# Optimization experiments

Measured on AMD Instinct MI355X. Metric: run time of the kernel, lower is better.

## Reference

```python
import jax, jax.numpy as jnp
import numpy as np

B, S, E, H, MAXLEN = 2, 2048, 1024, 16, 2048


def _level_indices(seq_len: int, base: int = 2) -> np.ndarray:
    """Vectorized version of get_level_index_weak over the full (target, source) grid.
    indices[t, s] = min(level, 2) for s < t, else 0. Runs in O(log S) passes."""
    tt = np.broadcast_to(np.arange(seq_len)[:, None], (seq_len, seq_len)).astype(np.int64).copy()
    ss = np.broadcast_to(np.arange(seq_len)[None, :], (seq_len, seq_len)).astype(np.int64).copy()
    res = np.zeros((seq_len, seq_len), np.int64)
    done = ~(ss < tt)  # only source < target positions get a level; rest stay 0
    while not done.all():
        l = np.floor(np.log2(np.maximum(tt, 1).astype(np.float64))).astype(np.int64)
        v = (np.int64(1) << l)
        hit = (~done) & (ss < v)
        res[hit] = l[hit] + 1
        done |= hit
        step = ~done
        tt[step] -= v[step]
        ss[step] -= v[step]
    return np.minimum(res, 2).astype(np.int32)


def setup_inputs() -> dict:
    key = jax.random.key(0)
    ks = jax.random.split(key, 10)
    sc = 0.02
    return {
        "x": jax.random.normal(ks[0], (B, S, E), dtype=jnp.float32),
        "attention_mask": jax.random.randint(ks[1], (B, S), 0, 2, dtype=jnp.int32),
        "level_indices": jnp.asarray(_level_indices(S, 2)),
        "Wq": jax.random.normal(ks[2], (E, E), dtype=jnp.float32) * sc,
        "bq": jnp.zeros((E,), jnp.float32),
        "Wk": jax.random.normal(ks[3], (E, E), dtype=jnp.float32) * sc,
        "bk": jnp.zeros((E,), jnp.float32),
        "Wv": jax.random.normal(ks[4], (E, E), dtype=jnp.float32) * sc,
        "bv": jnp.zeros((E,), jnp.float32),
        "hier": jax.random.normal(ks[5], (MAXLEN, H, 3), dtype=jnp.float32),
        "Wo": jax.random.normal(ks[6], (E, E), dtype=jnp.float32) * sc,
        "bo": jnp.zeros((E,), jnp.float32),
    }


def reference(x, attention_mask, level_indices, Wq, bq, Wk, bk, Wv, bv, hier, Wo, bo):
    b, s, e = x.shape
    h = hier.shape[1]
    dh = e // h
    # q/k are computed by the original module but never used; kept for fidelity (zero grads).
    q = x @ Wq.T + bq
    k = x @ Wk.T + bk
    v = (x @ Wv.T + bv).reshape(b, s, h, dh).transpose(0, 2, 1, 3)  # [B,H,S,Dh]
    lev = level_indices[:s, :s]  # [S,S] int, values in {0,1,2}
    # Faithful torch.gather semantics: weights[b,h,i,j] = hier[b, h, lev[i,j]]
    w3 = hier[:b]                      # [B,H,3]
    weights = w3[:, :, lev]            # [B,H,S,S]
    decay = jnp.power(jnp.float32(0.5), lev.astype(x.dtype))  # [S,S]
    weights = weights * decay
    weights = weights / (jnp.sum(weights, axis=-1, keepdims=True) + 1e-8)
    weights = jnp.where(attention_mask[:, None, None, :] == 0, jnp.float32(0.0), weights)
    out = jnp.einsum('bhij,bhjd->bhid', weights, v)  # [B,H,S,Dh]
    out = out.transpose(0, 2, 1, 3).reshape(b, s, e)
    return out @ Wo.T + bo
```

## Files before the change

kernel.cpp:

```cpp
#include <hip/hip_runtime.h>
#include <cstdint>
#include <cstddef>

constexpr int Sn = 2048;
constexpr int En = 1024;
constexpr int Bn = 2;
constexpr int Hn = 16;
constexpr int CHUNK = 64;
constexpr int NCH = Sn / CHUNK;
constexpr int Mtot = Bn * Sn;
constexpr int GCH = Mtot / CHUNK;
constexpr int KB = En / 32;

typedef __bf16 bf16x8 __attribute__((ext_vector_type(8)));
typedef float  f32x4  __attribute__((ext_vector_type(4)));

__device__ __forceinline__ unsigned short f2bf(float f) {
    union { float f; uint32_t u; } v; v.f = f;
    const uint32_t u = v.u;
    return (unsigned short)((u + 0x7fffu + ((u >> 16) & 1u)) >> 16);
}
__device__ __forceinline__ float bf2f(unsigned short s) {
    union { uint32_t u; float f; } v; v.u = (uint32_t)s << 16; return v.f;
}

__device__ __forceinline__ size_t swz_idx(int r, int c, int kb ) {
    const int blk = (r >> 4) * kb + (c >> 5);
    return (size_t)blk * 512 + (((r & 15) + (((c >> 3) & 3) << 4)) << 3) + (c & 7);
}

constexpr int XN = Bn * Sn * En;
constexpr int WN = En * En;

__global__ __launch_bounds__(256)
void cast3(const float* __restrict__ x, const float* __restrict__ Wv,
           const float* __restrict__ Wo, unsigned short* __restrict__ xb,
           unsigned short* __restrict__ Wvb, unsigned short* __restrict__ Wob)
{
    const int i = (blockIdx.x * 256 + threadIdx.x) * 4;
    const float* src; unsigned short* dst; int off;
    if (i < XN)           { src = x;  dst = xb;  off = i; }
    else if (i < XN + WN) { src = Wv; dst = Wvb; off = i - XN; }
    else                  { src = Wo; dst = Wob; off = i - XN - WN; }
    const float4 v = *(const float4*)(src + off);
    ushort4 o;
    o.x = f2bf(v.x); o.y = f2bf(v.y); o.z = f2bf(v.z); o.w = f2bf(v.w);
    const int r = off >> 10, c = off & 1023;
    *(ushort4*)(dst + swz_idx(r, c, KB)) = o;
}

template<bool APPLY_MASK, bool OUT_BF16, bool FUSE_CSUM>
__global__ __launch_bounds__(256)
void gemm_flat(const unsigned short* __restrict__ A, const unsigned short* __restrict__ Bw,
               const float* __restrict__ bias, const int* __restrict__ mask,
               void* __restrict__ Cv, float* __restrict__ csum)
{
    const int tid  = threadIdx.x;
    const int lane = tid & 63;
    const int wv   = tid >> 6;
    const int wr   = wv >> 1;
    const int wc   = wv & 1;
    const int id   = blockIdx.y * 16 + blockIdx.x;
    const int xcd  = id & 7;
    const int slot = id >> 3;
    const int by   = xcd * 4 + (slot >> 4);
    const int bx   = slot & 15;
    const int bm   = by * 128;
    const int bn   = bx * 64;
    const int m16  = lane & 15;
    const int kq   = lane >> 4;

    f32x4 acc[4][2] = {};

    const int rb = by * 8 + wr * 4;
    const int cb = bx * 4 + wc * 2;
    const unsigned short* aBase = A  + (size_t)rb * KB * 512 + lane * 8;
    const unsigned short* bBase = Bw + (size_t)cb * KB * 512 + lane * 8;

#pragma unroll 4
    for (int kc = 0; kc < KB; ++kc) {
        bf16x8 af0 = *(const bf16x8*)(aBase + (size_t)(0 * KB + kc) * 512);
        bf16x8 af1 = *(const bf16x8*)(aBase + (size_t)(1 * KB + kc) * 512);
        bf16x8 af2 = *(const bf16x8*)(aBase + (size_t)(2 * KB + kc) * 512);
        bf16x8 af3 = *(const bf16x8*)(aBase + (size_t)(3 * KB + kc) * 512);
        bf16x8 bf0 = *(const bf16x8*)(bBase + (size_t)(0 * KB + kc) * 512);
        bf16x8 bf1 = *(const bf16x8*)(bBase + (size_t)(1 * KB + kc) * 512);
        acc[0][0] = __builtin_amdgcn_mfma_f32_16x16x32_bf16(af0, bf0, acc[0][0], 0, 0, 0);
        acc[0][1] = __builtin_amdgcn_mfma_f32_16x16x32_bf16(af0, bf1, acc[0][1], 0, 0, 0);
        acc[1][0] = __builtin_amdgcn_mfma_f32_16x16x32_bf16(af1, bf0, acc[1][0], 0, 0, 0);
        acc[1][1] = __builtin_amdgcn_mfma_f32_16x16x32_bf16(af1, bf1, acc[1][1], 0, 0, 0);
        acc[2][0] = __builtin_amdgcn_mfma_f32_16x16x32_bf16(af2, bf0, acc[2][0], 0, 0, 0);
        acc[2][1] = __builtin_amdgcn_mfma_f32_16x16x32_bf16(af2, bf1, acc[2][1], 0, 0, 0);
        acc[3][0] = __builtin_amdgcn_mfma_f32_16x16x32_bf16(af3, bf0, acc[3][0], 0, 0, 0);
        acc[3][1] = __builtin_amdgcn_mfma_f32_16x16x32_bf16(af3, bf1, acc[3][1], 0, 0, 0);
    }

    float colsum[2] = {0.0f, 0.0f};
#pragma unroll
    for (int i = 0; i < 4; ++i) {
        const int r0 = bm + wr * 64 + i * 16 + kq * 4;
#pragma unroll
        for (int j = 0; j < 2; ++j) {
            const int c0 = bn + wc * 32 + j * 16 + m16;
            const float bcol = bias[c0];
#pragma unroll
            for (int r = 0; r < 4; ++r) {
                const int row = r0 + r;
                float val = acc[i][j][r] + bcol;
                if (APPLY_MASK) val = (mask[row] == 0) ? 0.0f : val;
                if (FUSE_CSUM) colsum[j] += val;
                if (OUT_BF16)
                    ((unsigned short*)Cv)[(size_t)row * En + c0] = f2bf(val);
                else
                    ((float*)Cv)[(size_t)row * En + c0] = val;
            }
        }
    }

    if (FUSE_CSUM) {
        const int gc = 2 * by + wr;
#pragma unroll
        for (int j = 0; j < 2; ++j) {
            float s = colsum[j];
            s += __shfl_xor(s, 16, 64);
            s += __shfl_xor(s, 32, 64);
            if (kq == 0)
                csum[(size_t)gc * En + bn + wc * 32 + j * 16 + m16] = s;
        }
    }
}

__global__ __launch_bounds__(256)
void combine(const unsigned short* __restrict__ vm, const float* __restrict__ csum,
             const float* __restrict__ hier, unsigned short* __restrict__ opre)
{
    const int e = blockIdx.x * 256 + threadIdx.x;
    const int c = blockIdx.y;
    const int b = blockIdx.z;
    const int h = e >> 6;

    const float w0 = hier[((size_t)b * Hn + h) * 3 + 0];
    const float w1 = hier[((size_t)b * Hn + h) * 3 + 1] * 0.5f;
    const float w2 = hier[((size_t)b * Hn + h) * 3 + 2] * 0.25f;

    float run = 0.0f, T = 0.0f;
    const int g0 = b * NCH;
    for (int c2 = 0; c2 < NCH; ++c2) {
        const float v = csum[(size_t)(g0 + c2) * En + e];
        if (c2 < c) run += v;
        T += v;
    }

    const int ecol  = (e >> 5);
    const int elane = ((e >> 3) & 3) << 4;
    const int epos  = e & 7;

    float prev = 0.0f;
    const size_t base = ((size_t)b * Sn + c * CHUNK) * En + e;

    for (int t = 0; t < CHUNK; ++t) {
        const int i = c * CHUNK + t;
        const float cur = bf2f(vm[base + (size_t)t * En]);
        float num, Z;
        if (i & 1) {
            num = w2 * (run - prev) + w1 * prev + w0 * (T - run);
            Z = (float)(i - 1) * w2 + w1 + (float)(Sn - i) * w0 + 1e-8f;
        } else {
            num = w2 * run + w0 * (T - run);
            Z = (float)i * w2 + (float)(Sn - i) * w0 + 1e-8f;
        }
        const int gi = b * Sn + i;
        const size_t di = (size_t)((gi >> 4) * KB + ecol) * 512
                        + ((((gi & 15) + elane)) << 3) + epos;
        opre[di] = f2bf(num / Z);
        run += cur;
        prev = cur;
    }
}

extern "C" void kernel_launch(void* const* d_in, const int* in_sizes, int n_in,
                              void* d_out, int out_size, void* d_ws, size_t ws_size,
                              hipStream_t stream)
{
    const float* x    = (const float*)d_in[0];
    const int*   mask = (const int*)d_in[1];
    const float* Wv   = (const float*)d_in[7];
    const float* bv   = (const float*)d_in[8];
    const float* hier = (const float*)d_in[9];
    const float* Wo   = (const float*)d_in[10];
    const float* bo   = (const float*)d_in[11];
    float* out = (float*)d_out;

    char* ws = (char*)d_ws;
    unsigned short* xb    = (unsigned short*)ws;  ws += (size_t)Mtot * En * 2;
    unsigned short* Wvb   = (unsigned short*)ws;  ws += (size_t)En * En * 2;
    unsigned short* Wob   = (unsigned short*)ws;  ws += (size_t)En * En * 2;
    unsigned short* vmb   = (unsigned short*)ws;  ws += (size_t)Mtot * En * 2;
    float*          csum  = (float*)ws;           ws += (size_t)GCH * En * 4;
    unsigned short* opreb = (unsigned short*)ws;  ws += (size_t)Mtot * En * 2;

    dim3 threads(256);

    cast3<<<dim3((XN + 2 * WN) / 1024), threads, 0, stream>>>(x, Wv, Wo, xb, Wvb, Wob);

    dim3 gemm_grid(16, 32);

    gemm_flat<true, true, true><<<gemm_grid, threads, 0, stream>>>(xb, Wvb, bv, mask, vmb, csum);
    combine<<<dim3(En / 256, NCH, Bn), threads, 0, stream>>>(vmb, csum, hier, opreb);
    gemm_flat<false, false, false><<<gemm_grid, threads, 0, stream>>>(opreb, Wob, bo, nullptr, out, nullptr);
}
```

Before: 180.3 us.

## Stage GEMM tiles through LDS with register prefetch, drop swizzled layout

Both GEMMs stop reading pre-swizzled fragments straight from global memory. They now load 128-wide K slabs from row-major bf16 buffers into registers, stage them into shared memory in MFMA fragment order, and prefetch the next slab while computing the current one. The cast and combine kernels now write plain row-major output instead of the swizzled layout. The aim is to share A/B tiles across waves and hide global latency, at the cost of extra barriers and 48KB of LDS per block, which may reduce occupancy.

```diff
diff --git a/kernel.cpp b/kernel.cpp
--- a/kernel.cpp
+++ b/kernel.cpp
@@ -10,7 +10,6 @@
 constexpr int NCH = Sn / CHUNK;
 constexpr int Mtot = Bn * Sn;
 constexpr int GCH = Mtot / CHUNK;
-constexpr int KB = En / 32;
 
 typedef __bf16 bf16x8 __attribute__((ext_vector_type(8)));
 typedef float  f32x4  __attribute__((ext_vector_type(4)));
@@ -22,11 +21,6 @@
 }
 __device__ __forceinline__ float bf2f(unsigned short s) {
     union { uint32_t u; float f; } v; v.u = (uint32_t)s << 16; return v.f;
-}
-
-__device__ __forceinline__ size_t swz_idx(int r, int c, int kb ) {
-    const int blk = (r >> 4) * kb + (c >> 5);
-    return (size_t)blk * 512 + (((r & 15) + (((c >> 3) & 3) << 4)) << 3) + (c & 7);
 }
 
 constexpr int XN = Bn * Sn * En;
@@ -45,16 +39,58 @@
     const float4 v = *(const float4*)(src + off);
     ushort4 o;
     o.x = f2bf(v.x); o.y = f2bf(v.y); o.z = f2bf(v.z); o.w = f2bf(v.w);
-    const int r = off >> 10, c = off & 1023;
-    *(ushort4*)(dst + swz_idx(r, c, KB)) = o;
-}
+    *(ushort4*)(dst + off) = o;
+}
+
+#define LOAD12(S, k0)                                \
+    S##a0 = *(const uint4*)(gA0 + (k0));             \
+    S##a1 = *(const uint4*)(gA0 + (k0) + 32);        \
+    S##a2 = *(const uint4*)(gA0 + (k0) + 64);        \
+    S##a3 = *(const uint4*)(gA0 + (k0) + 96);        \
+    S##a4 = *(const uint4*)(gA1 + (k0));             \
+    S##a5 = *(const uint4*)(gA1 + (k0) + 32);        \
+    S##a6 = *(const uint4*)(gA1 + (k0) + 64);        \
+    S##a7 = *(const uint4*)(gA1 + (k0) + 96);        \
+    S##b0 = *(const uint4*)(gB0 + (k0));             \
+    S##b1 = *(const uint4*)(gB0 + (k0) + 32);        \
+    S##b2 = *(const uint4*)(gB0 + (k0) + 64);        \
+    S##b3 = *(const uint4*)(gB0 + (k0) + 96);
+
+#define STORE12(S)                                   \
+    *lA0 = S##a0; *lA1 = S##a1; *lA2 = S##a2; *lA3 = S##a3; \
+    *lA4 = S##a4; *lA5 = S##a5; *lA6 = S##a6; *lA7 = S##a7; \
+    *lB0 = S##b0; *lB1 = S##b1; *lB2 = S##b2; *lB3 = S##b3;
+
+#define COMPUTE128()                                                                           \
+    {                                                                                          \
+        _Pragma("unroll")                                                                      \
+        for (int kh = 0; kh < 4; ++kh) {                                                       \
+            bf16x8 af0 = *(const bf16x8*)&As[((wr * 4 + 0) * 4 + kh) * 512 + lane * 8];        \
+            bf16x8 af1 = *(const bf16x8*)&As[((wr * 4 + 1) * 4 + kh) * 512 + lane * 8];        \
+            bf16x8 af2 = *(const bf16x8*)&As[((wr * 4 + 2) * 4 + kh) * 512 + lane * 8];        \
+            bf16x8 af3 = *(const bf16x8*)&As[((wr * 4 + 3) * 4 + kh) * 512 + lane * 8];        \
+            bf16x8 bf0 = *(const bf16x8*)&Bs[((wc * 2 + 0) * 4 + kh) * 512 + lane * 8];        \
+            bf16x8 bf1 = *(const bf16x8*)&Bs[((wc * 2 + 1) * 4 + kh) * 512 + lane * 8];        \
+            acc[0][0] = __builtin_amdgcn_mfma_f32_16x16x32_bf16(af0, bf0, acc[0][0], 0, 0, 0); \
+            acc[0][1] = __builtin_amdgcn_mfma_f32_16x16x32_bf16(af0, bf1, acc[0][1], 0, 0, 0); \
+            acc[1][0] = __builtin_amdgcn_mfma_f32_16x16x32_bf16(af1, bf0, acc[1][0], 0, 0, 0); \
+            acc[1][1] = __builtin_amdgcn_mfma_f32_16x16x32_bf16(af1, bf1, acc[1][1], 0, 0, 0); \
+            acc[2][0] = __builtin_amdgcn_mfma_f32_16x16x32_bf16(af2, bf0, acc[2][0], 0, 0, 0); \
+            acc[2][1] = __builtin_amdgcn_mfma_f32_16x16x32_bf16(af2, bf1, acc[2][1], 0, 0, 0); \
+            acc[3][0] = __builtin_amdgcn_mfma_f32_16x16x32_bf16(af3, bf0, acc[3][0], 0, 0, 0); \
+            acc[3][1] = __builtin_amdgcn_mfma_f32_16x16x32_bf16(af3, bf1, acc[3][1], 0, 0, 0); \
+        }                                                                                      \
+    }
 
 template<bool APPLY_MASK, bool OUT_BF16, bool FUSE_CSUM>
 __global__ __launch_bounds__(256)
-void gemm_flat(const unsigned short* __restrict__ A, const unsigned short* __restrict__ Bw,
-               const float* __restrict__ bias, const int* __restrict__ mask,
-               void* __restrict__ Cv, float* __restrict__ csum)
-{
+void gemm_bk128(const unsigned short* __restrict__ A, const unsigned short* __restrict__ Bw,
+                const float* __restrict__ bias, const int* __restrict__ mask,
+                void* __restrict__ Cv, float* __restrict__ csum)
+{
+    __shared__ __align__(16) unsigned short As[128 * 128];
+    __shared__ __align__(16) unsigned short Bs[64 * 128];
+
     const int tid  = threadIdx.x;
     const int lane = tid & 63;
     const int wv   = tid >> 6;
@@ -72,27 +108,41 @@
 
     f32x4 acc[4][2] = {};
 
-    const int rb = by * 8 + wr * 4;
-    const int cb = bx * 4 + wc * 2;
-    const unsigned short* aBase = A  + (size_t)rb * KB * 512 + lane * 8;
-    const unsigned short* bBase = Bw + (size_t)cb * KB * 512 + lane * 8;
-
-#pragma unroll 4
-    for (int kc = 0; kc < KB; ++kc) {
-        bf16x8 af0 = *(const bf16x8*)(aBase + (size_t)(0 * KB + kc) * 512);
-        bf16x8 af1 = *(const bf16x8*)(aBase + (size_t)(1 * KB + kc) * 512);
-        bf16x8 af2 = *(const bf16x8*)(aBase + (size_t)(2 * KB + kc) * 512);
-        bf16x8 af3 = *(const bf16x8*)(aBase + (size_t)(3 * KB + kc) * 512);
-        bf16x8 bf0 = *(const bf16x8*)(bBase + (size_t)(0 * KB + kc) * 512);
-        bf16x8 bf1 = *(const bf16x8*)(bBase + (size_t)(1 * KB + kc) * 512);
-        acc[0][0] = __builtin_amdgcn_mfma_f32_16x16x32_bf16(af0, bf0, acc[0][0], 0, 0, 0);
-        acc[0][1] = __builtin_amdgcn_mfma_f32_16x16x32_bf16(af0, bf1, acc[0][1], 0, 0, 0);
-        acc[1][0] = __builtin_amdgcn_mfma_f32_16x16x32_bf16(af1, bf0, acc[1][0], 0, 0, 0);
-        acc[1][1] = __builtin_amdgcn_mfma_f32_16x16x32_bf16(af1, bf1, acc[1][1], 0, 0, 0);
-        acc[2][0] = __builtin_amdgcn_mfma_f32_16x16x32_bf16(af2, bf0, acc[2][0], 0, 0, 0);
-        acc[2][1] = __builtin_amdgcn_mfma_f32_16x16x32_bf16(af2, bf1, acc[2][1], 0, 0, 0);
-        acc[3][0] = __builtin_amdgcn_mfma_f32_16x16x32_bf16(af3, bf0, acc[3][0], 0, 0, 0);
-        acc[3][1] = __builtin_amdgcn_mfma_f32_16x16x32_bf16(af3, bf1, acc[3][1], 0, 0, 0);
+    const int rg0 = 2 * wv, rg1 = 2 * wv + 1;
+    const unsigned short* gA0 = A  + (size_t)(bm + 16 * rg0 + m16) * En + kq * 8;
+    const unsigned short* gA1 = A  + (size_t)(bm + 16 * rg1 + m16) * En + kq * 8;
+    const unsigned short* gB0 = Bw + (size_t)(bn + 16 * wv  + m16) * En + kq * 8;
+    uint4* lA0 = (uint4*)&As[(rg0 * 4 + 0) * 512 + lane * 8];
+    uint4* lA1 = (uint4*)&As[(rg0 * 4 + 1) * 512 + lane * 8];
+    uint4* lA2 = (uint4*)&As[(rg0 * 4 + 2) * 512 + lane * 8];
+    uint4* lA3 = (uint4*)&As[(rg0 * 4 + 3) * 512 + lane * 8];
+    uint4* lA4 = (uint4*)&As[(rg1 * 4 + 0) * 512 + lane * 8];
+    uint4* lA5 = (uint4*)&As[(rg1 * 4 + 1) * 512 + lane * 8];
+    uint4* lA6 = (uint4*)&As[(rg1 * 4 + 2) * 512 + lane * 8];
+    uint4* lA7 = (uint4*)&As[(rg1 * 4 + 3) * 512 + lane * 8];
+    uint4* lB0 = (uint4*)&Bs[(wv * 4 + 0) * 512 + lane * 8];
+    uint4* lB1 = (uint4*)&Bs[(wv * 4 + 1) * 512 + lane * 8];
+    uint4* lB2 = (uint4*)&Bs[(wv * 4 + 2) * 512 + lane * 8];
+    uint4* lB3 = (uint4*)&Bs[(wv * 4 + 3) * 512 + lane * 8];
+
+    uint4 pa0, pa1, pa2, pa3, pa4, pa5, pa6, pa7, pb0, pb1, pb2, pb3;
+    uint4 qa0, qa1, qa2, qa3, qa4, qa5, qa6, qa7, qb0, qb1, qb2, qb3;
+
+    LOAD12(p, 0);
+#pragma unroll 1
+    for (int it = 0; it < 4; ++it) {
+        const int kbase = it * 256;
+        __syncthreads();
+        STORE12(p);
+        __syncthreads();
+        LOAD12(q, kbase + 128);
+        COMPUTE128();
+
+        __syncthreads();
+        STORE12(q);
+        __syncthreads();
+        if (it < 3) { LOAD12(p, kbase + 256); }
+        COMPUTE128();
     }
 
     float colsum[2] = {0.0f, 0.0f};
@@ -151,10 +201,6 @@
         T += v;
     }
 
-    const int ecol  = (e >> 5);
-    const int elane = ((e >> 3) & 3) << 4;
-    const int epos  = e & 7;
-
     float prev = 0.0f;
     const size_t base = ((size_t)b * Sn + c * CHUNK) * En + e;
 
@@ -169,10 +215,7 @@
             num = w2 * run + w0 * (T - run);
             Z = (float)i * w2 + (float)(Sn - i) * w0 + 1e-8f;
         }
-        const int gi = b * Sn + i;
-        const size_t di = (size_t)((gi >> 4) * KB + ecol) * 512
-                        + ((((gi & 15) + elane)) << 3) + epos;
-        opre[di] = f2bf(num / Z);
+        opre[base + (size_t)t * En] = f2bf(num / Z);
         run += cur;
         prev = cur;
     }
@@ -205,7 +248,7 @@
 
     dim3 gemm_grid(16, 32);
 
-    gemm_flat<true, true, true><<<gemm_grid, threads, 0, stream>>>(xb, Wvb, bv, mask, vmb, csum);
+    gemm_bk128<true, true, true><<<gemm_grid, threads, 0, stream>>>(xb, Wvb, bv, mask, vmb, csum);
     combine<<<dim3(En / 256, NCH, Bn), threads, 0, stream>>>(vmb, csum, hier, opreb);
-    gemm_flat<false, false, false><<<gemm_grid, threads, 0, stream>>>(opreb, Wob, bo, nullptr, out, nullptr);
-}
+    gemm_bk128<false, false, false><<<gemm_grid, threads, 0, stream>>>(opreb, Wob, bo, nullptr, out, nullptr);
+}
```

Result: faster. 171.4 us (-5.0%).
